# Kernel tuning notes

Hardware: AMD Instinct MI355X
Metric: run time of the kernel (lower is better)

Reference implementation:

```python
import jax, jax.numpy as jnp
import numpy as np

BS = 128          # block size hard-coded in linear_deepseek_v3
FP8_MAX = 448.0   # float8_e4m3fn max-normal, used by act_quant_deepseek_v3


def act_quant(x):
    """Per-token, per-128-column-block activation quantization.
    x: [T, K] -> (xq [T, K], scale [T, K//BS]) with xq = x / scale per block."""
    T, K = x.shape
    xb = x.reshape(T, K // BS, BS)
    amax = jnp.max(jnp.abs(xb), axis=-1)              # [T, K//BS]
    scale = amax / FP8_MAX + 1e-12
    xq = (xb / scale[:, :, None]).reshape(T, K)
    return xq, scale


def linear_dsv3(x, wq, w_scale):
    """y = dequant(act_quant(x)) @ dequant(wq, w_scale).T
    x: [T, K]; wq: [N, K] fp8-style values; w_scale: [N//BS, K//BS]."""
    T, K = x.shape
    N = wq.shape[0]
    xq, xs = act_quant(x)
    # dequantized activations [T, K]
    xdq = (xq.reshape(T, K // BS, BS) * xs[:, :, None]).reshape(T, K)
    # dequantized weights [N, K] via 128x128 block scales
    wdq = (wq.reshape(N // BS, BS, K // BS, BS) * w_scale[:, None, :, None]).reshape(N, K)
    return xdq @ wdq.T


def setup_inputs() -> dict:
    key = jax.random.key(0)
    ks = jax.random.split(key, 4)
    DIM, INTER = 4096, 14336

    def make_qweight(k, n, m):
        w = jax.random.normal(k, (n, m), dtype=jnp.float32) * 0.02
        wb = w.reshape(n // BS, BS, m // BS, BS)
        amax = jnp.max(jnp.abs(wb), axis=(1, 3))       # [n//BS, m//BS]
        scale = amax / FP8_MAX + 1e-12
        wq = (wb / scale[:, None, :, None]).reshape(n, m)
        return wq, scale

    x = jax.random.normal(ks[0], (2, 1024, DIM), dtype=jnp.float32)
    w1, w1_scale = make_qweight(ks[1], INTER, DIM)
    w3, w3_scale = make_qweight(ks[2], INTER, DIM)
    w2, w2_scale = make_qweight(ks[3], DIM, INTER)
    return {"x": x, "w1": w1, "w1_scale": w1_scale, "w3": w3,
            "w3_scale": w3_scale, "w2": w2, "w2_scale": w2_scale}


def reference(x, w1, w1_scale, w3, w3_scale, w2, w2_scale):
    B, S, D = x.shape
    xf = x.reshape(-1, D)                               # [T, D]
    g = linear_dsv3(xf, w1, w1_scale)                   # gate  [T, INTER]
    u = linear_dsv3(xf, w3, w3_scale)                   # up    [T, INTER]
    h = jax.nn.silu(g) * u                              # SwiGLU
    y = linear_dsv3(h, w2, w2_scale)                    # down  [T, D]
    return y.reshape(B, S, D)
```

## Files before the change

### kernel.cpp

```cpp
#include <hip/hip_runtime.h>
#include <hip/hip_bf16.h>
#include <stdint.h>

typedef __attribute__((ext_vector_type(8))) short short8;
typedef __attribute__((ext_vector_type(4))) float f32x4;
typedef __attribute__((ext_vector_type(8))) unsigned short u16x8;

static __device__ __forceinline__ unsigned short f2bf(float f) {
  union { float f; unsigned int u; } c; c.f = f;
  unsigned int u = c.u;
  u += 0x7FFFu + ((u >> 16) & 1u);
  return (unsigned short)(u >> 16);
}
static __device__ __forceinline__ float bf2f(unsigned short h) {
  union { unsigned int u; float f; } c; c.u = ((unsigned int)h) << 16;
  return c.f;
}
static __device__ __forceinline__ f32x4 mfma_bf16(short8 a, short8 b, f32x4 c) {
  return __builtin_amdgcn_mfma_f32_16x16x32_bf16(a, b, c, 0, 0, 0);
}
static __device__ __forceinline__ void gl_lds16(const void* g, void* lds) {
  __builtin_amdgcn_global_load_lds(
      (const __attribute__((address_space(1))) void*)(unsigned long long)(uintptr_t)g,
      (__attribute__((address_space(3))) void*)(unsigned int)(uintptr_t)lds,
      16, 0, 0);
}

__global__ void k_cvt_w(const float* __restrict__ w, const float* __restrict__ s,
                        unsigned short* __restrict__ o, int N, int K) {
  const int KB = K >> 7;
  const size_t total = ((size_t)N * K) >> 3;
  for (size_t i = (size_t)blockIdx.x * blockDim.x + threadIdx.x; i < total;
       i += (size_t)gridDim.x * blockDim.x) {
    const size_t e = i << 3;
    const int n = (int)(e / K);
    const int k = (int)(e % K);
    const float sc = s[(n >> 7) * KB + (k >> 7)];
    f32x4 a = *(const f32x4*)(w + e);
    f32x4 b = *(const f32x4*)(w + e + 4);
    u16x8 q;
    #pragma unroll
    for (int j = 0; j < 4; ++j) { q[j] = f2bf(a[j] * sc); q[4 + j] = f2bf(b[j] * sc); }
    *(u16x8*)(o + e) = q;
  }
}

__global__ void k_cvt_x(const float* __restrict__ x, unsigned short* __restrict__ o,
                        size_t total8) {
  for (size_t i = (size_t)blockIdx.x * blockDim.x + threadIdx.x; i < total8;
       i += (size_t)gridDim.x * blockDim.x) {
    const size_t e = i << 3;
    f32x4 a = *(const f32x4*)(x + e);
    f32x4 b = *(const f32x4*)(x + e + 4);
    u16x8 q;
    #pragma unroll
    for (int j = 0; j < 4; ++j) { q[j] = f2bf(a[j]); q[4 + j] = f2bf(b[j]); }
    *(u16x8*)(o + e) = q;
  }
}

#define PH_MID() do { \
    __builtin_amdgcn_sched_barrier(0); \
    __builtin_amdgcn_s_barrier(); \
    asm volatile("s_waitcnt lgkmcnt(0)" ::: "memory"); \
    __builtin_amdgcn_sched_barrier(0); \
    __builtin_amdgcn_s_setprio(1); \
  } while (0)
#define PH_END() do { \
    __builtin_amdgcn_s_setprio(0); \
    __builtin_amdgcn_sched_barrier(0); \
    __builtin_amdgcn_s_barrier(); \
  } while (0)

#define READ_A(d, mh) do { \
    const char* _ba = (const char*)lds + ((d) * 2 + wm) * 16384; \
    _Pragma("unroll") \
    for (int f = 0; f < 4; ++f) { \
      aF[0][f] = *(const short8*)(_ba + ((((mh) * 64 + f * 16 + lr) * 128 + kg * 16) ^ xr)); \
      aF[1][f] = *(const short8*)(_ba + ((((mh) * 64 + f * 16 + lr) * 128 + 64 + kg * 16) ^ xr)); \
    } } while (0)
#define READ_B(d, nh, bF) do { \
    const char* _bb = (const char*)lds + ABYTES + ((d) * NBH + bhalf) * 16384; \
    _Pragma("unroll") \
    for (int f = 0; f < NH2; ++f) { \
      bF[0][f] = *(const short8*)(_bb + (((wrow0 + ((nh) * NH2 + f) * 16 + lr) * 128 + kg * 16) ^ xr)); \
      bF[1][f] = *(const short8*)(_bb + (((wrow0 + ((nh) * NH2 + f) * 16 + lr) * 128 + 64 + kg * 16) ^ xr)); \
    } } while (0)
#define MFMA_Q(mh, nh, bF) do { \
    _Pragma("unroll") \
    for (int m = 0; m < 4; ++m) \
      _Pragma("unroll") \
      for (int n = 0; n < NH2; ++n) { \
        acc[(mh) * 4 + m][(nh) * NH2 + n] = \
            mfma_bf16(aF[0][m], bF[0][n], acc[(mh) * 4 + m][(nh) * NH2 + n]); \
        acc[(mh) * 4 + m][(nh) * NH2 + n] = \
            mfma_bf16(aF[1][m], bF[1][n], acc[(mh) * 4 + m][(nh) * NH2 + n]); \
      } } while (0)

template<int NB, int EPI>
__global__ __launch_bounds__(512, 2)
void k_gemm8p(const unsigned short* __restrict__ A,
              const unsigned short* __restrict__ B,
              const unsigned short* Gin,
              void* Out,
              int M, int N, int K) {
  constexpr int BN     = NB * 128;
  constexpr int NREP   = NB * 2;
  constexpr int NH2    = NREP / 2;
  constexpr int NBH    = NB;
  constexpr int ABYTES = 65536;
  __shared__ unsigned short lds[(NB == 2) ? 65536 : 49152];

  const int tid  = threadIdx.x;
  const int lane = tid & 63;
  const int wid  = tid >> 6;
  const int wm   = wid >> 2;
  const int wn   = wid & 3;
  const int lr   = lane & 15;
  const int kg   = lane >> 4;
  const int xr   = (lr & 7) << 4;

  const int nwg = gridDim.x;
  const int per = nwg >> 3;
  const int wg  = (int)blockIdx.x;
  const int swz = (wg & 7) * per + (wg >> 3);
  const int bm  = swz & 7;
  const int bn  = swz >> 3;

  const int r0   = tid >> 3;
  const int colb = ((tid & 7) ^ ((tid >> 3) & 7)) << 4;
  const size_t ldb = (size_t)K * 2;

  const char* gA = (const char*)A + (size_t)bm * 256 * ldb;
  const char* gB = (const char*)B + (size_t)bn * BN * ldb;

  const int wrow0 = (NB == 2) ? (wn & 1) * 64 : wn * 32;
  const int bhalf = (NB == 2) ? (wn >> 1) : 0;

  auto stageA = [&](int t, int h) {
    unsigned short* d = lds + ((t & 1) * 2 + h) * 8192 + wid * 512;
    const char* s = gA + (size_t)(h * 128 + r0) * ldb + (size_t)t * 128 + colb;
    gl_lds16(s, d);
    gl_lds16(s + 64 * ldb, d + 4096);
  };
  auto stageB = [&](int t, int h) {
    unsigned short* d = lds + (ABYTES / 2) + ((t & 1) * NBH + h) * 8192 + wid * 512;
    const char* s = gB + (size_t)(h * 128 + r0) * ldb + (size_t)t * 128 + colb;
    gl_lds16(s, d);
    gl_lds16(s + 64 * ldb, d + 4096);
  };

  f32x4 acc[8][NREP];
  #pragma unroll
  for (int m = 0; m < 8; ++m)
    #pragma unroll
    for (int n = 0; n < NREP; ++n)
      #pragma unroll
      for (int e = 0; e < 4; ++e) acc[m][n][e] = 0.0f;

  short8 aF[2][4], bF0[2][NH2], bF1[2][NH2];

  const int NP = K >> 7;

  stageB(0, 0); if constexpr (NB == 2) stageB(0, 1);
  stageA(0, 0); stageA(0, 1);
  stageB(1, 0); if constexpr (NB == 2) stageB(1, 1);
  stageA(1, 0); stageA(1, 1);
  if constexpr (NB == 2) asm volatile("s_waitcnt vmcnt(8)" ::: "memory");
  else                   asm volatile("s_waitcnt vmcnt(6)" ::: "memory");
  __builtin_amdgcn_sched_barrier(0);
  __builtin_amdgcn_s_barrier();

  for (int i = 0; i < NP; ++i) {
    const int t0 = 2 * i, t1 = 2 * i + 1;
    const bool more = (i + 1 < NP);

    READ_A(0, 0);
    READ_B(0, 0, bF0);
    if (i > 0) stageA(t1, 1);
    PH_MID(); MFMA_Q(0, 0, bF0); PH_END();

    READ_B(0, 1, bF1);
    PH_MID(); MFMA_Q(0, 1, bF1); PH_END();

    READ_A(0, 1);
    if (more) stageB(t0 + 2, 0);
    PH_MID(); MFMA_Q(1, 1, bF1); PH_END();

    if (more) { if constexpr (NB == 2) stageB(t0 + 2, 1); stageA(t0 + 2, 0); }
    PH_MID(); MFMA_Q(1, 0, bF0);
    __builtin_amdgcn_s_setprio(0);
    __builtin_amdgcn_sched_barrier(0);
    if (more) {
      if constexpr (NB == 2) asm volatile("s_waitcnt vmcnt(6)" ::: "memory");
      else                   asm volatile("s_waitcnt vmcnt(4)" ::: "memory");
    } else {
      asm volatile("s_waitcnt vmcnt(0)" ::: "memory");
    }
    __builtin_amdgcn_sched_barrier(0);
    __builtin_amdgcn_s_barrier();

    READ_A(1, 0);
    READ_B(1, 0, bF0);
    if (more) stageA(t0 + 2, 1);
    PH_MID(); MFMA_Q(0, 0, bF0); PH_END();

    READ_B(1, 1, bF1);
    PH_MID(); MFMA_Q(0, 1, bF1); PH_END();

    READ_A(1, 1);
    if (more) stageB(t1 + 2, 0);
    PH_MID(); MFMA_Q(1, 1, bF1); PH_END();

    if (more) { if constexpr (NB == 2) stageB(t1 + 2, 1); stageA(t1 + 2, 0); }
    PH_MID(); MFMA_Q(1, 0, bF0);
    __builtin_amdgcn_s_setprio(0);
    __builtin_amdgcn_sched_barrier(0);
    if (more) {
      if constexpr (NB == 2) asm volatile("s_waitcnt vmcnt(6)" ::: "memory");
      else                   asm volatile("s_waitcnt vmcnt(4)" ::: "memory");
    }
    __builtin_amdgcn_sched_barrier(0);
    __builtin_amdgcn_s_barrier();
  }

  const int growb = bm * 256 + wm * 128 + kg * 4;
  const int gcolb = bn * BN + wn * (BN / 4) + lr;
  #pragma unroll
  for (int m = 0; m < 8; ++m)
    #pragma unroll
    for (int n = 0; n < NREP; ++n)
      #pragma unroll
      for (int j = 0; j < 4; ++j) {
        const size_t idx = (size_t)(growb + m * 16 + j) * N + (gcolb + n * 16);
        if constexpr (EPI == 0) {
          ((unsigned short*)Out)[idx] = f2bf(acc[m][n][j]);
        } else if constexpr (EPI == 1) {
          const float gv = bf2f(Gin[idx]);
          const float sg = gv / (1.0f + __expf(-gv));
          ((unsigned short*)Out)[idx] = f2bf(sg * acc[m][n][j]);
        } else {
          ((float*)Out)[idx] = acc[m][n][j];
        }
      }
}

extern "C" void kernel_launch(void* const* d_in, const int* in_sizes, int n_in,
                              void* d_out, int out_size, void* d_ws, size_t ws_size,
                              hipStream_t stream) {
  const float* x   = (const float*)d_in[0];
  const float* w1  = (const float*)d_in[1];
  const float* w1s = (const float*)d_in[2];
  const float* w3  = (const float*)d_in[3];
  const float* w3s = (const float*)d_in[4];
  const float* w2  = (const float*)d_in[5];
  const float* w2s = (const float*)d_in[6];
  float* y = (float*)d_out;

  const int D = 4096, I = 14336;
  const int T = in_sizes[0] / D;

  const size_t xbB = (size_t)T * D * 2;
  const size_t wB  = (size_t)I * D * 2;

  char* ws = (char*)d_ws;
  unsigned short* xb  = (unsigned short*)(ws);
  unsigned short* w1b = (unsigned short*)(ws + xbB);
  unsigned short* w3b = (unsigned short*)(ws + xbB + wB);
  unsigned short* w2b = (unsigned short*)(ws + xbB + 2 * wB);
  unsigned short* g   = (unsigned short*)(ws + xbB + 3 * wB);

  k_cvt_x<<<2048, 256, 0, stream>>>(x, xb, ((size_t)T * D) >> 3);
  k_cvt_w<<<2048, 256, 0, stream>>>(w1, w1s, w1b, I, D);
  k_cvt_w<<<2048, 256, 0, stream>>>(w3, w3s, w3b, I, D);
  k_cvt_w<<<2048, 256, 0, stream>>>(w2, w2s, w2b, D, I);

  k_gemm8p<2, 0><<<dim3((T / 256) * (I / 256)), dim3(512), 0, stream>>>(
      xb, w1b, nullptr, g, T, I, D);
  k_gemm8p<2, 1><<<dim3((T / 256) * (I / 256)), dim3(512), 0, stream>>>(
      xb, w3b, g, g, T, I, D);
  k_gemm8p<1, 2><<<dim3((T / 256) * (D / 128)), dim3(512), 0, stream>>>(
      g, w2b, nullptr, y, T, D, I);
}
```

Before: 938.3 us.

## Software-pipeline LDS fragment reads across MFMA phases with partial lgkmcnt waits

```diff
diff --git a/kernel.cpp b/kernel.cpp
--- a/kernel.cpp
+++ b/kernel.cpp
@@ -59,42 +59,34 @@
   }
 }
 
-#define PH_MID() do { \
-    __builtin_amdgcn_sched_barrier(0); \
-    __builtin_amdgcn_s_barrier(); \
-    asm volatile("s_waitcnt lgkmcnt(0)" ::: "memory"); \
-    __builtin_amdgcn_sched_barrier(0); \
-    __builtin_amdgcn_s_setprio(1); \
-  } while (0)
-#define PH_END() do { \
-    __builtin_amdgcn_s_setprio(0); \
-    __builtin_amdgcn_sched_barrier(0); \
-    __builtin_amdgcn_s_barrier(); \
-  } while (0)
-
-#define READ_A(d, mh) do { \
-    const char* _ba = (const char*)lds + ((d) * 2 + wm) * 16384; \
+#define SB  __builtin_amdgcn_sched_barrier(0)
+#define BAR __builtin_amdgcn_s_barrier()
+#define LGKM(n) asm volatile("s_waitcnt lgkmcnt(%0)" :: "n"(n) : "memory")
+#define VMC(n)  asm volatile("s_waitcnt vmcnt(%0)"  :: "n"(n) : "memory")
+#define MID(n) do { SB; BAR; LGKM(n); SB; __builtin_amdgcn_s_setprio(1); } while (0)
+#define ENDP() do { __builtin_amdgcn_s_setprio(0); SB; BAR; } while (0)
+
+#define RD_A(slot, mh, dst) do { \
+    const char* _ba = (const char*)lds + ((slot) * 2 + wm) * 16384; \
     _Pragma("unroll") \
     for (int f = 0; f < 4; ++f) { \
-      aF[0][f] = *(const short8*)(_ba + ((((mh) * 64 + f * 16 + lr) * 128 + kg * 16) ^ xr)); \
-      aF[1][f] = *(const short8*)(_ba + ((((mh) * 64 + f * 16 + lr) * 128 + 64 + kg * 16) ^ xr)); \
+      dst[0][f] = *(const short8*)(_ba + ((((mh) * 64 + f * 16 + lr) * 128 + kg * 16) ^ xr)); \
+      dst[1][f] = *(const short8*)(_ba + ((((mh) * 64 + f * 16 + lr) * 128 + 64 + kg * 16) ^ xr)); \
     } } while (0)
-#define READ_B(d, nh, bF) do { \
-    const char* _bb = (const char*)lds + ABYTES + ((d) * NBH + bhalf) * 16384; \
+#define RD_B(slot, nh, dst) do { \
+    const char* _bb = (const char*)lds + ABYTES + ((slot) * NBH + bhalf) * 16384; \
     _Pragma("unroll") \
     for (int f = 0; f < NH2; ++f) { \
-      bF[0][f] = *(const short8*)(_bb + (((wrow0 + ((nh) * NH2 + f) * 16 + lr) * 128 + kg * 16) ^ xr)); \
-      bF[1][f] = *(const short8*)(_bb + (((wrow0 + ((nh) * NH2 + f) * 16 + lr) * 128 + 64 + kg * 16) ^ xr)); \
+      dst[0][f] = *(const short8*)(_bb + (((wrow0 + ((nh) * NH2 + f) * 16 + lr) * 128 + kg * 16) ^ xr)); \
+      dst[1][f] = *(const short8*)(_bb + (((wrow0 + ((nh) * NH2 + f) * 16 + lr) * 128 + 64 + kg * 16) ^ xr)); \
     } } while (0)
-#define MFMA_Q(mh, nh, bF) do { \
+#define MF(aS, bS, mh, nh) do { \
     _Pragma("unroll") \
     for (int m = 0; m < 4; ++m) \
       _Pragma("unroll") \
       for (int n = 0; n < NH2; ++n) { \
-        acc[(mh) * 4 + m][(nh) * NH2 + n] = \
-            mfma_bf16(aF[0][m], bF[0][n], acc[(mh) * 4 + m][(nh) * NH2 + n]); \
-        acc[(mh) * 4 + m][(nh) * NH2 + n] = \
-            mfma_bf16(aF[1][m], bF[1][n], acc[(mh) * 4 + m][(nh) * NH2 + n]); \
+        acc[(mh)*4+m][(nh)*NH2+n] = mfma_bf16(aS[0][m], bS[0][n], acc[(mh)*4+m][(nh)*NH2+n]); \
+        acc[(mh)*4+m][(nh)*NH2+n] = mfma_bf16(aS[1][m], bS[1][n], acc[(mh)*4+m][(nh)*NH2+n]); \
       } } while (0)
 
 template<int NB, int EPI>
@@ -109,6 +101,11 @@
   constexpr int NH2    = NREP / 2;
   constexpr int NBH    = NB;
   constexpr int ABYTES = 65536;
+  constexpr int LG0    = 2 * NH2;
+  constexpr int LG1    = 8;
+  constexpr int LG3    = 8 + 2 * NH2;
+  constexpr int VMN    = (NB == 2) ? 6 : 4;
+  constexpr int VPR    = (NB == 2) ? 8 : 6;
   __shared__ unsigned short lds[(NB == 2) ? 65536 : 49152];
 
   const int tid  = threadIdx.x;
@@ -158,70 +155,55 @@
       #pragma unroll
       for (int e = 0; e < 4; ++e) acc[m][n][e] = 0.0f;
 
-  short8 aF[2][4], bF0[2][NH2], bF1[2][NH2];
-
-  const int NP = K >> 7;
-
-  stageB(0, 0); if constexpr (NB == 2) stageB(0, 1);
-  stageA(0, 0); stageA(0, 1);
-  stageB(1, 0); if constexpr (NB == 2) stageB(1, 1);
-  stageA(1, 0); stageA(1, 1);
-  if constexpr (NB == 2) asm volatile("s_waitcnt vmcnt(8)" ::: "memory");
-  else                   asm volatile("s_waitcnt vmcnt(6)" ::: "memory");
-  __builtin_amdgcn_sched_barrier(0);
-  __builtin_amdgcn_s_barrier();
+  short8 aS0[2][4], aS1[2][4], bX[2][NH2], bY[2][NH2];
+
+  const int NT = K >> 6;
+  const int NP = NT >> 1;
+
+  stageA(0, 0); stageA(0, 1); stageB(0, 0); if constexpr (NB == 2) stageB(0, 1);
+  stageA(1, 0); stageA(1, 1); stageB(1, 0); if constexpr (NB == 2) stageB(1, 1);
+  VMC(VPR); SB; BAR;
+  RD_A(0, 0, aS0);
+  RD_B(0, 0, bX);
 
   for (int i = 0; i < NP; ++i) {
-    const int t0 = 2 * i, t1 = 2 * i + 1;
+    const int t0 = 2 * i;
     const bool more = (i + 1 < NP);
 
-    READ_A(0, 0);
-    READ_B(0, 0, bF0);
-    if (i > 0) stageA(t1, 1);
-    PH_MID(); MFMA_Q(0, 0, bF0); PH_END();
-
-    READ_B(0, 1, bF1);
-    PH_MID(); MFMA_Q(0, 1, bF1); PH_END();
-
-    READ_A(0, 1);
-    if (more) stageB(t0 + 2, 0);
-    PH_MID(); MFMA_Q(1, 1, bF1); PH_END();
-
-    if (more) { if constexpr (NB == 2) stageB(t0 + 2, 1); stageA(t0 + 2, 0); }
-    PH_MID(); MFMA_Q(1, 0, bF0);
-    __builtin_amdgcn_s_setprio(0);
-    __builtin_amdgcn_sched_barrier(0);
+    RD_B(0, 1, bY);
+    MID(LG0); MF(aS0, bX, 0, 0); ENDP();
+    RD_A(0, 1, aS1);
+    if (more) { stageA(t0 + 2, 0); stageB(t0 + 2, 0); }
+    MID(LG1); MF(aS0, bY, 0, 1); ENDP();
+    if (more) { if constexpr (NB == 2) stageB(t0 + 2, 1); }
+    MID(0); MF(aS1, bY, 1, 1);
+    __builtin_amdgcn_s_setprio(0); SB;
+    if (more) { VMC(VMN); } else { VMC(0); }
+    SB; BAR;
+    RD_A(1, 0, aS0);
+    RD_B(1, 0, bY);
+    if (more) stageA(t0 + 2, 1);
+    MID(LG3); MF(aS1, bX, 1, 0); ENDP();
+
+    RD_B(1, 1, bX);
+    MID(LG0); MF(aS0, bY, 0, 0); ENDP();
+    RD_A(1, 1, aS1);
+    if (more) { stageA(t0 + 3, 0); stageB(t0 + 3, 0); }
+    MID(LG1); MF(aS0, bX, 0, 1); ENDP();
+    if (more) { if constexpr (NB == 2) stageB(t0 + 3, 1); }
+    MID(0); MF(aS1, bX, 1, 1);
+    __builtin_amdgcn_s_setprio(0); SB;
+    if (more) { VMC(VMN); } else { VMC(0); }
+    SB; BAR;
     if (more) {
-      if constexpr (NB == 2) asm volatile("s_waitcnt vmcnt(6)" ::: "memory");
-      else                   asm volatile("s_waitcnt vmcnt(4)" ::: "memory");
+      RD_A(0, 0, aS0);
+      RD_B(0, 0, bX);
+      stageA(t0 + 3, 1);
+      MID(LG3);
     } else {
-      asm volatile("s_waitcnt vmcnt(0)" ::: "memory");
+      MID(0);
     }
-    __builtin_amdgcn_sched_barrier(0);
-    __builtin_amdgcn_s_barrier();
-
-    READ_A(1, 0);
-    READ_B(1, 0, bF0);
-    if (more) stageA(t0 + 2, 1);
-    PH_MID(); MFMA_Q(0, 0, bF0); PH_END();
-
-    READ_B(1, 1, bF1);
-    PH_MID(); MFMA_Q(0, 1, bF1); PH_END();
-
-    READ_A(1, 1);
-    if (more) stageB(t1 + 2, 0);
-    PH_MID(); MFMA_Q(1, 1, bF1); PH_END();
-
-    if (more) { if constexpr (NB == 2) stageB(t1 + 2, 1); stageA(t1 + 2, 0); }
-    PH_MID(); MFMA_Q(1, 0, bF0);
-    __builtin_amdgcn_s_setprio(0);
-    __builtin_amdgcn_sched_barrier(0);
-    if (more) {
-      if constexpr (NB == 2) asm volatile("s_waitcnt vmcnt(6)" ::: "memory");
-      else                   asm volatile("s_waitcnt vmcnt(4)" ::: "memory");
-    }
-    __builtin_amdgcn_sched_barrier(0);
-    __builtin_amdgcn_s_barrier();
+    MF(aS1, bY, 1, 0); ENDP();
   }
 
   const int growb = bm * 256 + wm * 128 + kg * 4;
```

Result: slower. 1.792 ms (+91.0%).
